# Optimization experiments

Hardware: AMD Instinct MI355X
Metric: run time of the kernel (lower is better)

The kernel has to match this reference:

```python
import jax, jax.numpy as jnp
import numpy as np

GROUPS = 52
B, C, H, W = 16, 52, 256, 256  # c must equal groups (see t_value.view(b, c, 1, 1) in source)


def setup_inputs() -> dict:
    key = jax.random.key(0)
    ks = jax.random.split(key, 4)
    x = jax.random.normal(ks[0], (B, C, H, W), jnp.float32)
    weight = jax.random.normal(ks[1], (1, GROUPS, 1, 1), jnp.float32) * 0.1
    bias = jnp.ones((1, GROUPS, 1, 1), jnp.float32)
    one = jnp.ones((1, GROUPS, 1), jnp.float32)
    zero = jax.random.normal(ks[2], (1, GROUPS, 1), jnp.float32) * 0.1
    theta = jax.random.uniform(ks[3], (1, 2, 1, 1), jnp.float32)
    scale = jnp.ones((1,), jnp.float32)
    return dict(x=x, weight=weight, bias=bias, one=one, zero=zero, theta=theta, scale=scale)


def _prm_forward(x, weight, bias, one, zero, theta, scale):
    b, c, h, w = x.shape
    G = GROUPS
    cpg = c // G  # == 1 (required by original code)
    bg, hw = b * G, h * w

    xv = x.reshape(bg, cpg, hw)                      # [bg, cpg, hw]
    value = xv.sum(axis=1)                           # per-group channel-sum map [bg, hw]

    # adaptive max pool with indices (row-major argmax, first occurrence, same as torch)
    idx = jnp.argmax(value, axis=1)                  # [bg]
    qrow = (idx // w).astype(x.dtype)                # [bg]
    qcol = (idx % w).astype(x.dtype)                 # [bg]
    qval = jnp.take_along_axis(value, idx[:, None], axis=1)  # [bg, 1] == query_value

    # tiny per-group similarity matmuls (contraction over cpg)
    sim_max = jnp.einsum('gc,gch->gh', qval, xv)     # [bg, hw]
    gap = x.mean(axis=(2, 3)).reshape(bg, cpg)       # global avg pool per group-channel
    sim_gap = jnp.einsum('gc,gch->gh', gap, xv)      # [bg, hw]

    # positional Gaussian weighting: Normal(0, scale).log_prob(d * theta).exp()
    sigma = scale[0]
    log_norm = -jnp.log(sigma) - 0.5 * jnp.log(2.0 * jnp.pi)

    def gpdf(z):
        return jnp.exp(-0.5 * (z / sigma) ** 2 + log_norm)

    rows = jnp.arange(h, dtype=x.dtype)
    cols = jnp.arange(w, dtype=x.dtype)
    dr = jnp.abs(rows[None, :, None] - qrow[:, None, None])   # [bg, h, 1]
    dc = jnp.abs(cols[None, None, :] - qcol[:, None, None])   # [bg, 1, w]
    # mean over the 2 coordinate channels; broadcast avoids materializing [bg,2,h,w]
    dist = 0.5 * (gpdf(dr * theta[0, 0, 0, 0]) + gpdf(dc * theta[0, 1, 0, 0]))  # [bg, h, w]

    sim_max = sim_max.reshape(b, G, hw) * dist.reshape(b, G, hw)
    sim_gap = sim_gap.reshape(b, G, hw)
    sim = sim_max * zero + sim_gap * one             # [b, G, hw]

    # spatial mean/std normalization (torch .std -> ddof=1)
    ctx = sim - sim.mean(axis=2, keepdims=True)
    std = jnp.std(ctx, axis=2, keepdims=True, ddof=1) + 1e-05
    ctx = (ctx / std).reshape(b, G, h, w) * weight + bias

    # broadcast per-group gate over the group's channels, then sigmoid gate
    ctx = jnp.broadcast_to(ctx.reshape(bg, 1, h, w), (bg, cpg, h, w)).reshape(b, c, h, w)
    return x * jax.nn.sigmoid(ctx)


def reference(x, weight, bias, one, zero, theta, scale):
    return _prm_forward(x, weight, bias, one, zero, theta, scale)
```

## Files before the change

### kernel.cpp

```cpp
#include <hip/hip_runtime.h>
#include <math.h>

#define Bn 16
#define Gn 52
#define Hn 256
#define Wn 256
#define HW (Hn * Wn)
#define HW4 (HW / 4)
#define BG (Bn * Gn)


__global__ __launch_bounds__(256) void k_reduce1(const float4* __restrict__ x4,
                                                 float* __restrict__ ws) {
    const int bg = blockIdx.x;
    const int t = threadIdx.x;
    const size_t base4 = (size_t)bg * HW4;

    float vmax = -INFINITY;
    int imax = 0;
    float sum = 0.f;
    for (int i = t; i < HW4; i += 256) {
        float4 v = x4[base4 + i];
        sum += (v.x + v.y) + (v.z + v.w);
        int e = i * 4;
        if (v.x > vmax) { vmax = v.x; imax = e; }
        if (v.y > vmax) { vmax = v.y; imax = e + 1; }
        if (v.z > vmax) { vmax = v.z; imax = e + 2; }
        if (v.w > vmax) { vmax = v.w; imax = e + 3; }
    }

    __shared__ float sv[256];
    __shared__ int   si[256];
    __shared__ float ss[256];
    sv[t] = vmax; si[t] = imax; ss[t] = sum;
    __syncthreads();
    for (int s = 128; s > 0; s >>= 1) {
        if (t < s) {
            ss[t] += ss[t + s];
            float ov = sv[t + s]; int oi = si[t + s];
            if (ov > sv[t] || (ov == sv[t] && oi < si[t])) { sv[t] = ov; si[t] = oi; }
        }
        __syncthreads();
    }
    if (t == 0) {
        ws[bg]          = sv[0];
        ws[BG + bg]     = (float)(si[0] >> 8);
        ws[2 * BG + bg] = (float)(si[0] & 255);
        ws[3 * BG + bg] = ss[0] * (1.f / (float)HW);
    }
}

__global__ __launch_bounds__(256) void k_stats(const float4* __restrict__ x4,
                                               const float* __restrict__ weight,
                                               const float* __restrict__ one_,
                                               const float* __restrict__ zero,
                                               const float* __restrict__ theta,
                                               const float* __restrict__ scale,
                                               float* __restrict__ ws) {
    const int bg = blockIdx.x;
    const int g = bg % Gn;
    const int t = threadIdx.x;
    const size_t base4 = (size_t)bg * HW4;

    const float qval = ws[bg];
    const float qrow = ws[BG + bg];
    const float qcol = ws[2 * BG + bg];
    const float gap  = ws[3 * BG + bg];
    const float A  = zero[g] * qval;
    const float Bc = one_[g] * gap;
    const float th0 = theta[0], th1 = theta[1];
    const float sigma = scale[0];
    const float inv2s2 = 0.5f / (sigma * sigma);
    const float lognorm = -logf(sigma) - 0.9189385332046727f;

    float s1 = 0.f, s2 = 0.f;
    for (int i = t; i < HW4; i += 256) {
        float4 v = x4[base4 + i];
        int e = i * 4;
        float r = (float)(e >> 8);
        float c = (float)(e & 255);
        float zr = (r - qrow) * th0;
        float gr = __expf(lognorm - zr * zr * inv2s2);
        #pragma unroll
        for (int j = 0; j < 4; ++j) {
            float vj = (j == 0) ? v.x : (j == 1) ? v.y : (j == 2) ? v.z : v.w;
            float zc = (c + (float)j - qcol) * th1;
            float gc = __expf(lognorm - zc * zc * inv2s2);
            float dist = 0.5f * (gr + gc);
            float sim = (A * dist + Bc) * vj;
            s1 += sim;
            s2 += sim * sim;
        }
    }

    __shared__ float a1[256];
    __shared__ float a2[256];
    a1[t] = s1; a2[t] = s2;
    __syncthreads();
    for (int s = 128; s > 0; s >>= 1) {
        if (t < s) { a1[t] += a1[t + s]; a2[t] += a2[t + s]; }
        __syncthreads();
    }
    if (t == 0) {
        float S1 = a1[0], S2 = a2[0];
        float mean = S1 * (1.f / (float)HW);
        float var = (S2 - S1 * mean) / (float)(HW - 1);
        var = fmaxf(var, 0.f);
        float std_ = sqrtf(var);
        float inv = 1.f / (std_ + 1e-5f);
        ws[4 * BG + bg] = mean;
        ws[5 * BG + bg] = weight[g] * inv;
    }
}

__global__ __launch_bounds__(256) void k_out(const float4* __restrict__ x4,
                                             const float* __restrict__ bias,
                                             const float* __restrict__ one_,
                                             const float* __restrict__ zero,
                                             const float* __restrict__ theta,
                                             const float* __restrict__ scale,
                                             const float* __restrict__ ws,
                                             float4* __restrict__ out4) {
    const int bg = blockIdx.y;
    const int g = bg % Gn;
    const size_t base4 = (size_t)bg * HW4;

    const float qval = ws[bg];
    const float qrow = ws[BG + bg];
    const float qcol = ws[2 * BG + bg];
    const float gap  = ws[3 * BG + bg];
    const float mean = ws[4 * BG + bg];
    const float wsc  = ws[5 * BG + bg];
    const float A  = zero[g] * qval;
    const float Bc = one_[g] * gap;
    const float bb = bias[g];
    const float th0 = theta[0], th1 = theta[1];
    const float sigma = scale[0];
    const float inv2s2 = 0.5f / (sigma * sigma);
    const float lognorm = -logf(sigma) - 0.9189385332046727f;

    int i0 = blockIdx.x * 1024 + threadIdx.x;
    #pragma unroll
    for (int it = 0; it < 4; ++it) {
        int i = i0 + it * 256;
        float4 v = x4[base4 + i];
        int e = i * 4;
        float r = (float)(e >> 8);
        float c = (float)(e & 255);
        float zr = (r - qrow) * th0;
        float gr = __expf(lognorm - zr * zr * inv2s2);
        float4 o;
        #pragma unroll
        for (int j = 0; j < 4; ++j) {
            float vj = (j == 0) ? v.x : (j == 1) ? v.y : (j == 2) ? v.z : v.w;
            float zc = (c + (float)j - qcol) * th1;
            float gc = __expf(lognorm - zc * zc * inv2s2);
            float dist = 0.5f * (gr + gc);
            float sim = (A * dist + Bc) * vj;
            float ctx = (sim - mean) * wsc + bb;
            float sg = __builtin_amdgcn_rcpf(1.0f + __expf(-ctx));
            float oj = vj * sg;
            if (j == 0) o.x = oj; else if (j == 1) o.y = oj; else if (j == 2) o.z = oj; else o.w = oj;
        }
        out4[base4 + i] = o;
    }
}

extern "C" void kernel_launch(void* const* d_in, const int* in_sizes, int n_in,
                              void* d_out, int out_size, void* d_ws, size_t ws_size,
                              hipStream_t stream) {
    const float* x      = (const float*)d_in[0];
    const float* weight = (const float*)d_in[1];
    const float* bias   = (const float*)d_in[2];
    const float* one_   = (const float*)d_in[3];
    const float* zero   = (const float*)d_in[4];
    const float* theta  = (const float*)d_in[5];
    const float* scale  = (const float*)d_in[6];
    float* out = (float*)d_out;
    float* ws  = (float*)d_ws;

    const float4* x4 = (const float4*)x;
    float4* out4 = (float4*)out;

    k_reduce1<<<BG, 256, 0, stream>>>(x4, ws);
    k_stats<<<BG, 256, 0, stream>>>(x4, weight, one_, zero, theta, scale, ws);
    k_out<<<dim3(16, BG), 256, 0, stream>>>(x4, bias, one_, zero, theta, scale, ws, out4);
}
```

Measured before the change: 443.4 us.

## Fuse three passes into one register-resident kernel per group

Merges the argmax/mean reduction, the statistics pass and the output pass into one kernel. Each 1024-thread block loads its whole 64K-element group map into registers once and reuses it for all three phases. This removes two extra full reads of x, two launches and the workspace round trip. It also replaces shared-memory tree reductions with wave shuffles. The cost is heavy register use per thread, low occupancy and no overlap between memory and compute inside a block.

```diff
diff --git a/kernel.cpp b/kernel.cpp
--- a/kernel.cpp
+++ b/kernel.cpp
@@ -1,168 +1,141 @@
 #include <hip/hip_runtime.h>
 #include <math.h>
 
-#define Bn 16
 #define Gn 52
 #define Hn 256
 #define Wn 256
 #define HW (Hn * Wn)
 #define HW4 (HW / 4)
-#define BG (Bn * Gn)
+#define BG 832
+#define TPB 1024
+#define VPT 16
 
+__global__ __launch_bounds__(TPB) void k_fused(
+    const float4* __restrict__ x4,
+    const float* __restrict__ weight, const float* __restrict__ bias,
+    const float* __restrict__ one_,  const float* __restrict__ zero,
+    const float* __restrict__ theta, const float* __restrict__ scale,
+    float4* __restrict__ out4)
+{
+    const int bg   = blockIdx.x;
+    const int g    = bg % Gn;
+    const int t    = threadIdx.x;
+    const int wave = t >> 6;
+    const int lane = t & 63;
+    const size_t base4 = (size_t)bg * HW4;
+    const float4* xp = x4 + base4;
 
-__global__ __launch_bounds__(256) void k_reduce1(const float4* __restrict__ x4,
-                                                 float* __restrict__ ws) {
-    const int bg = blockIdx.x;
-    const int t = threadIdx.x;
-    const size_t base4 = (size_t)bg * HW4;
+    float4 v[VPT];
+    #pragma unroll
+    for (int k = 0; k < VPT; ++k) v[k] = xp[t + k * TPB];
 
-    float vmax = -INFINITY;
-    int imax = 0;
-    float sum = 0.f;
-    for (int i = t; i < HW4; i += 256) {
-        float4 v = x4[base4 + i];
-        sum += (v.x + v.y) + (v.z + v.w);
-        int e = i * 4;
-        if (v.x > vmax) { vmax = v.x; imax = e; }
-        if (v.y > vmax) { vmax = v.y; imax = e + 1; }
-        if (v.z > vmax) { vmax = v.z; imax = e + 2; }
-        if (v.w > vmax) { vmax = v.w; imax = e + 3; }
+    float vmax = -INFINITY; int imax = 0; float sum = 0.f;
+    #pragma unroll
+    for (int k = 0; k < VPT; ++k) {
+        int e = (t + k * TPB) * 4;
+        float4 q = v[k];
+        sum += (q.x + q.y) + (q.z + q.w);
+        if (q.x > vmax) { vmax = q.x; imax = e; }
+        if (q.y > vmax) { vmax = q.y; imax = e + 1; }
+        if (q.z > vmax) { vmax = q.z; imax = e + 2; }
+        if (q.w > vmax) { vmax = q.w; imax = e + 3; }
     }
+    #pragma unroll
+    for (int off = 32; off > 0; off >>= 1) {
+        float ov = __shfl_down(vmax, off);
+        int   oi = __shfl_down(imax, off);
+        float os = __shfl_down(sum,  off);
+        sum += os;
+        if (ov > vmax || (ov == vmax && oi < imax)) { vmax = ov; imax = oi; }
+    }
+    __shared__ float rv[16];
+    __shared__ int   ri[16];
+    __shared__ float r1[16];
+    __shared__ float r2[16];
+    __shared__ float bc[6];
+    if (lane == 0) { rv[wave] = vmax; ri[wave] = imax; r1[wave] = sum; }
+    __syncthreads();
+    if (t == 0) {
+        float bv = rv[0]; int bi = ri[0]; float bs = r1[0];
+        for (int i = 1; i < 16; ++i) {
+            bs += r1[i];
+            float ov = rv[i]; int oi = ri[i];
+            if (ov > bv || (ov == bv && oi < bi)) { bv = ov; bi = oi; }
+        }
+        bc[0] = bv;
+        bc[1] = (float)(bi >> 8);
+        bc[2] = (float)(bi & 255);
+        bc[3] = bs * (1.f / (float)HW);
+    }
+    __syncthreads();
 
-    __shared__ float sv[256];
-    __shared__ int   si[256];
-    __shared__ float ss[256];
-    sv[t] = vmax; si[t] = imax; ss[t] = sum;
-    __syncthreads();
-    for (int s = 128; s > 0; s >>= 1) {
-        if (t < s) {
-            ss[t] += ss[t + s];
-            float ov = sv[t + s]; int oi = si[t + s];
-            if (ov > sv[t] || (ov == sv[t] && oi < si[t])) { sv[t] = ov; si[t] = oi; }
-        }
-        __syncthreads();
-    }
-    if (t == 0) {
-        ws[bg]          = sv[0];
-        ws[BG + bg]     = (float)(si[0] >> 8);
-        ws[2 * BG + bg] = (float)(si[0] & 255);
-        ws[3 * BG + bg] = ss[0] * (1.f / (float)HW);
-    }
-}
-
-__global__ __launch_bounds__(256) void k_stats(const float4* __restrict__ x4,
-                                               const float* __restrict__ weight,
-                                               const float* __restrict__ one_,
-                                               const float* __restrict__ zero,
-                                               const float* __restrict__ theta,
-                                               const float* __restrict__ scale,
-                                               float* __restrict__ ws) {
-    const int bg = blockIdx.x;
-    const int g = bg % Gn;
-    const int t = threadIdx.x;
-    const size_t base4 = (size_t)bg * HW4;
-
-    const float qval = ws[bg];
-    const float qrow = ws[BG + bg];
-    const float qcol = ws[2 * BG + bg];
-    const float gap  = ws[3 * BG + bg];
-    const float A  = zero[g] * qval;
-    const float Bc = one_[g] * gap;
+    const float sigma   = scale[0];
+    const float inv2s2  = 0.5f / (sigma * sigma);
+    const float lognorm = -logf(sigma) - 0.9189385332046727f;
     const float th0 = theta[0], th1 = theta[1];
-    const float sigma = scale[0];
-    const float inv2s2 = 0.5f / (sigma * sigma);
-    const float lognorm = -logf(sigma) - 0.9189385332046727f;
+    const float qrow = bc[1], qcol = bc[2];
+    const float A  = zero[g] * bc[0];
+    const float Bc = one_[g] * bc[3];
 
     float s1 = 0.f, s2 = 0.f;
-    for (int i = t; i < HW4; i += 256) {
-        float4 v = x4[base4 + i];
-        int e = i * 4;
+    #pragma unroll
+    for (int k = 0; k < VPT; ++k) {
+        int e = (t + k * TPB) * 4;
         float r = (float)(e >> 8);
         float c = (float)(e & 255);
         float zr = (r - qrow) * th0;
         float gr = __expf(lognorm - zr * zr * inv2s2);
+        float4 q = v[k];
         #pragma unroll
         for (int j = 0; j < 4; ++j) {
-            float vj = (j == 0) ? v.x : (j == 1) ? v.y : (j == 2) ? v.z : v.w;
+            float vj = (j == 0) ? q.x : (j == 1) ? q.y : (j == 2) ? q.z : q.w;
             float zc = (c + (float)j - qcol) * th1;
             float gc = __expf(lognorm - zc * zc * inv2s2);
-            float dist = 0.5f * (gr + gc);
-            float sim = (A * dist + Bc) * vj;
+            float sim = (A * (0.5f * (gr + gc)) + Bc) * vj;
             s1 += sim;
             s2 += sim * sim;
         }
     }
+    #pragma unroll
+    for (int off = 32; off > 0; off >>= 1) {
+        s1 += __shfl_down(s1, off);
+        s2 += __shfl_down(s2, off);
+    }
+    if (lane == 0) { r1[wave] = s1; r2[wave] = s2; }
+    __syncthreads();
+    if (t == 0) {
+        float S1 = 0.f, S2 = 0.f;
+        for (int i = 0; i < 16; ++i) { S1 += r1[i]; S2 += r2[i]; }
+        float mean = S1 * (1.f / (float)HW);
+        float var  = (S2 - S1 * mean) * (1.f / (float)(HW - 1));
+        var = fmaxf(var, 0.f);
+        bc[4] = mean;
+        bc[5] = weight[g] / (sqrtf(var) + 1e-5f);
+    }
+    __syncthreads();
+    const float mean = bc[4], wsc = bc[5], bb = bias[g];
 
-    __shared__ float a1[256];
-    __shared__ float a2[256];
-    a1[t] = s1; a2[t] = s2;
-    __syncthreads();
-    for (int s = 128; s > 0; s >>= 1) {
-        if (t < s) { a1[t] += a1[t + s]; a2[t] += a2[t + s]; }
-        __syncthreads();
-    }
-    if (t == 0) {
-        float S1 = a1[0], S2 = a2[0];
-        float mean = S1 * (1.f / (float)HW);
-        float var = (S2 - S1 * mean) / (float)(HW - 1);
-        var = fmaxf(var, 0.f);
-        float std_ = sqrtf(var);
-        float inv = 1.f / (std_ + 1e-5f);
-        ws[4 * BG + bg] = mean;
-        ws[5 * BG + bg] = weight[g] * inv;
-    }
-}
-
-__global__ __launch_bounds__(256) void k_out(const float4* __restrict__ x4,
-                                             const float* __restrict__ bias,
-                                             const float* __restrict__ one_,
-                                             const float* __restrict__ zero,
-                                             const float* __restrict__ theta,
-                                             const float* __restrict__ scale,
-                                             const float* __restrict__ ws,
-                                             float4* __restrict__ out4) {
-    const int bg = blockIdx.y;
-    const int g = bg % Gn;
-    const size_t base4 = (size_t)bg * HW4;
-
-    const float qval = ws[bg];
-    const float qrow = ws[BG + bg];
-    const float qcol = ws[2 * BG + bg];
-    const float gap  = ws[3 * BG + bg];
-    const float mean = ws[4 * BG + bg];
-    const float wsc  = ws[5 * BG + bg];
-    const float A  = zero[g] * qval;
-    const float Bc = one_[g] * gap;
-    const float bb = bias[g];
-    const float th0 = theta[0], th1 = theta[1];
-    const float sigma = scale[0];
-    const float inv2s2 = 0.5f / (sigma * sigma);
-    const float lognorm = -logf(sigma) - 0.9189385332046727f;
-
-    int i0 = blockIdx.x * 1024 + threadIdx.x;
     #pragma unroll
-    for (int it = 0; it < 4; ++it) {
-        int i = i0 + it * 256;
-        float4 v = x4[base4 + i];
-        int e = i * 4;
+    for (int k = 0; k < VPT; ++k) {
+        int e = (t + k * TPB) * 4;
         float r = (float)(e >> 8);
         float c = (float)(e & 255);
         float zr = (r - qrow) * th0;
         float gr = __expf(lognorm - zr * zr * inv2s2);
-        float4 o;
+        float4 q = v[k], o;
         #pragma unroll
         for (int j = 0; j < 4; ++j) {
-            float vj = (j == 0) ? v.x : (j == 1) ? v.y : (j == 2) ? v.z : v.w;
+            float vj = (j == 0) ? q.x : (j == 1) ? q.y : (j == 2) ? q.z : q.w;
             float zc = (c + (float)j - qcol) * th1;
             float gc = __expf(lognorm - zc * zc * inv2s2);
-            float dist = 0.5f * (gr + gc);
-            float sim = (A * dist + Bc) * vj;
+            float sim = (A * (0.5f * (gr + gc)) + Bc) * vj;
             float ctx = (sim - mean) * wsc + bb;
-            float sg = __builtin_amdgcn_rcpf(1.0f + __expf(-ctx));
-            float oj = vj * sg;
-            if (j == 0) o.x = oj; else if (j == 1) o.y = oj; else if (j == 2) o.z = oj; else o.w = oj;
+            float sg  = __builtin_amdgcn_rcpf(1.f + __expf(-ctx));
+            float oj  = vj * sg;
+            if (j == 0) o.x = oj; else if (j == 1) o.y = oj;
+            else if (j == 2) o.z = oj; else o.w = oj;
         }
-        out4[base4 + i] = o;
+        out4[base4 + t + k * TPB] = o;
     }
 }
 
@@ -177,12 +150,7 @@
     const float* theta  = (const float*)d_in[5];
     const float* scale  = (const float*)d_in[6];
     float* out = (float*)d_out;
-    float* ws  = (float*)d_ws;
 
-    const float4* x4 = (const float4*)x;
-    float4* out4 = (float4*)out;
-
-    k_reduce1<<<BG, 256, 0, stream>>>(x4, ws);
-    k_stats<<<BG, 256, 0, stream>>>(x4, weight, one_, zero, theta, scale, ws);
-    k_out<<<dim3(16, BG), 256, 0, stream>>>(x4, bias, one_, zero, theta, scale, ws, out4);
+    k_fused<<<BG, TPB, 0, stream>>>((const float4*)x, weight, bias, one_, zero,
+                                    theta, scale, (float4*)out);
 }
```

New measurement: 407.3 us. 8.1% less time.
